# Performance work log

Measured on AMD Instinct MI355X. Metric: run time of the kernel, lower is better.

The kernel has to match this reference:

```python
import jax, jax.numpy as jnp
import numpy as np
import math

N_PATCH = 32768
DIM = 512
L_TOK = 64
W_SIZE = 64
STRIDE = 32


def setup_inputs() -> dict:
    key = jax.random.key(0)
    ks = jax.random.split(key, 12)
    d = DIM
    inp = {
        'feats': jax.random.normal(ks[0], (N_PATCH, d), dtype=jnp.float32),
        'coords': jax.random.uniform(ks[1], (N_PATCH, 2), dtype=jnp.float32),
        'mask': jnp.zeros((N_PATCH,), dtype=bool),
        'z': jax.random.normal(ks[2], (L_TOK, d), dtype=jnp.float32),
        'Wq': jax.random.normal(ks[3], (d, d), dtype=jnp.float32) / math.sqrt(d),
        'Wk': jax.random.normal(ks[4], (d, d), dtype=jnp.float32) / math.sqrt(d),
        'Wv': jax.random.normal(ks[5], (d, d), dtype=jnp.float32) / math.sqrt(d),
        'w1': jax.random.normal(ks[6], (d, 2), dtype=jnp.float32) / math.sqrt(2.0),
        'b1': jnp.zeros((d,), dtype=jnp.float32),
        'w2': jax.random.normal(ks[7], (d, d), dtype=jnp.float32) / math.sqrt(d),
        'b2': jnp.zeros((d,), dtype=jnp.float32),
        'Wo': jax.random.normal(ks[8], (d, d), dtype=jnp.float32) / math.sqrt(d),
        'bo': jnp.zeros((d,), dtype=jnp.float32),
    }
    return inp


def _lstcwa(feats, coords, z, Wq, Wk, Wv, w1, b1, w2, b2, Wo, bo):
    # mask is all-False -> feats kept as-is; N divisible by L -> equal segments
    N, D = feats.shape
    L = z.shape[0]
    n = N // L                       # patches per segment
    nwin = -(-n // STRIDE)           # windows per segment (ceil)

    # window offsets within a segment, [nwin, w]; last window truncated via mask
    off = jnp.arange(nwin)[:, None] * STRIDE + jnp.arange(W_SIZE)[None, :]
    valid = off < n                  # [nwin, w]
    idx = jnp.arange(L)[:, None, None] * n + jnp.minimum(off, n - 1)[None]  # [L,nwin,w]

    q = z @ Wq.T                     # [L, D]
    kf = feats @ Wk.T                # [N, D]
    vf = feats @ Wv.T

    k_win = kf[idx]                  # [L, nwin, w, D]
    v_win = vf[idx]
    c_win = coords[idx]              # [L, nwin, w, 2]

    vf32 = valid.astype(feats.dtype)                      # [nwin, w]
    cnt = vf32.sum(-1)                                    # [nwin]
    c_mean = jnp.einsum('lnwc,nw->lnc', c_win, vf32) / cnt[None, :, None]
    delta = (c_win - c_mean[:, :, None, :]) * vf32[None, :, :, None]

    pos = jax.nn.relu(delta @ w1.T + b1) @ w2.T + b2      # [L, nwin, w, D]
    k_win = k_win + pos

    logits = jnp.einsum('ld,lnwd->lnw', q, k_win) / math.sqrt(D)
    logits = jnp.where(valid[None], logits, -1e9)
    attn = jax.nn.softmax(logits, axis=-1)                # [L, nwin, w]

    z_win = jnp.einsum('lnw,lnwd->lnd', attn, v_win)      # [L, nwin, D]
    # return_alpha=False path: z_l_acc / max(1, len(attn_acc)=0) -> SUM over windows
    Z = z_win.sum(1)                                      # [L, D]
    return Z @ Wo.T + bo


def reference(feats, coords, mask, z, Wq, Wk, Wv, w1, b1, w2, b2, Wo, bo):
    # mask is all-False by construction (static shapes under jit)
    return _lstcwa(feats, coords, z, Wq, Wk, Wv, w1, b1, w2, b2, Wo, bo)
```

## Files before the change

kernel.cpp:

```cpp
#include <hip/hip_runtime.h>
#include <math.h>

#define DIMV 512
#define LTOK 64
#define SEG  512
#define NWIN 16
#define WSZ  64
#define INV_SQRT_D 0.044194173824159216f

__device__ __forceinline__ float wave_sum(float v) {
#pragma unroll
  for (int m = 1; m < 64; m <<= 1) v += __shfl_xor(v, m, 64);
  return v;
}

__global__ __launch_bounds__(256, 4) void k_q(const float* __restrict__ z,
    const float* __restrict__ Wq, const float* __restrict__ coords,
    float* __restrict__ q, float* __restrict__ cmean)
{
  int l = blockIdx.x >> 4, c = blockIdx.x & 15;
  int wave = threadIdx.x >> 6, lane = threadIdx.x & 63;
  int e0 = lane << 3;
  const float* zp = z + l * DIMV + e0;
  float x0[8];
  *(float4*)&x0[0] = *(const float4*)zp;
  *(float4*)&x0[4] = *(const float4*)(zp + 4);
  int d0 = c * 32 + wave * 8;
  float rf[8][8];
#pragma unroll
  for (int k = 0; k < 8; ++k) {
    const float* rp = Wq + (size_t)(d0 + k) * DIMV + e0;
    *(float4*)&rf[k][0] = *(const float4*)rp;
    *(float4*)&rf[k][4] = *(const float4*)(rp + 4);
  }
#pragma unroll
  for (int k = 0; k < 8; ++k) {
    float p = 0.f;
#pragma unroll
    for (int j = 0; j < 8; ++j) p = fmaf(rf[k][j], x0[j], p);
    p = wave_sum(p);
    if (lane == k) q[l * DIMV + d0 + k] = p;
  }
  if (wave == 0) {
    int n = c;
    int nvalid = (n == 15) ? 32 : 64;
    bool v = lane < nvalid;
    float cx = 0.f, cy = 0.f;
    if (v) {
      const float* cp = coords + ((size_t)(l * SEG + n * 32 + lane)) * 2;
      cx = cp[0]; cy = cp[1];
    }
    float inv = 1.0f / (float)nvalid;
    float mx = wave_sum(cx) * inv;
    float my = wave_sum(cy) * inv;
    if (lane == 0) {
      cmean[(l * NWIN + n) * 2]     = mx;
      cmean[(l * NWIN + n) * 2 + 1] = my;
    }
  }
}

__global__ __launch_bounds__(256) void k_qproj(const float* __restrict__ q,
    const float* __restrict__ Wk, const float* __restrict__ w2,
    const float* __restrict__ b2, float* __restrict__ qk,
    float* __restrict__ qw2, float* __restrict__ qb2)
{
  int l = blockIdx.x >> 3, ec = blockIdx.x & 7;
  int wave = threadIdx.x >> 6, lane = threadIdx.x & 63;
  int t = threadIdx.x;
  __shared__ float qs[DIMV];
  __shared__ float pk[4][64], pw[4][64];
  qs[t] = q[l * DIMV + t];
  qs[t + 256] = q[l * DIMV + t + 256];
  __syncthreads();
  int e = ec * 64 + lane;
  int d0 = wave * 128;
  float ak = 0.f, aw = 0.f;
#pragma unroll 8
  for (int dd = 0; dd < 128; ++dd) {
    int d = d0 + dd;
    float qd = qs[d];
    ak = fmaf(qd, Wk[(size_t)d * DIMV + e], ak);
    aw = fmaf(qd, w2[(size_t)d * DIMV + e], aw);
  }
  pk[wave][lane] = ak;
  pw[wave][lane] = aw;
  __syncthreads();
  if (wave == 0) {
    qk[l * DIMV + e] = pk[0][lane] + pk[1][lane] + pk[2][lane] + pk[3][lane];
  } else if (wave == 1) {
    qw2[l * DIMV + e] = pw[0][lane] + pw[1][lane] + pw[2][lane] + pw[3][lane];
  } else if (wave == 2 && ec == 0) {
    int e0 = lane << 3;
    float pb = 0.f;
#pragma unroll
    for (int j = 0; j < 8; ++j) pb = fmaf(qs[e0 + j], b2[e0 + j], pb);
    pb = wave_sum(pb);
    if (lane == 0) qb2[l] = pb;
  }
}

__global__ __launch_bounds__(256, 4) void k_pos(
    const float* __restrict__ coords, const float* __restrict__ cmean,
    const float* __restrict__ qw2,   const float* __restrict__ qb2,
    const float* __restrict__ w1,    const float* __restrict__ b1,
    float* __restrict__ pos)
{
  int widx = blockIdx.x;
  int l = widx >> 4, n = widx & 15;
  int t = threadIdx.x;
  int p = t & 63, qd = t >> 6;
  __shared__ float w1s[2 * DIMV], b1s[DIMV], qws[DIMV], part[4][WSZ];
#pragma unroll
  for (int i = 0; i < 4; ++i) w1s[t + 256 * i] = w1[t + 256 * i];
#pragma unroll
  for (int i = 0; i < 2; ++i) {
    b1s[t + 256 * i] = b1[t + 256 * i];
    qws[t + 256 * i] = qw2[l * DIMV + t + 256 * i];
  }
  __syncthreads();
  int nvalid = (n == 15) ? 32 : 64;
  int off = n * 32 + p;
  int row = (p < nvalid) ? off : (SEG - 1);
  float dx = coords[((size_t)(l * SEG + row)) * 2]     - cmean[(l * NWIN + n) * 2];
  float dy = coords[((size_t)(l * SEG + row)) * 2 + 1] - cmean[(l * NWIN + n) * 2 + 1];
  float acc = 0.f;
  int d0 = qd * 128;
#pragma unroll 4
  for (int dd = 0; dd < 128; ++dd) {
    int d = d0 + dd;
    float h = fmaf(dx, w1s[2 * d], fmaf(dy, w1s[2 * d + 1], b1s[d]));
    acc = fmaf(fmaxf(h, 0.f), qws[d], acc);
  }
  part[qd][p] = acc;
  __syncthreads();
  if (t < 64) {
    pos[(size_t)widx * WSZ + p] =
        part[0][p] + part[1][p] + part[2][p] + part[3][p] + qb2[l];
  }
}

__global__ __launch_bounds__(256, 4) void k_stream(
    const float* __restrict__ feats, const float* __restrict__ qk,
    const float* __restrict__ pos,   float* __restrict__ numA,
    float* __restrict__ numB, float* __restrict__ denA, float* __restrict__ denB)
{
  int bid = blockIdx.x;
  int swz = (bid & 7) * 128 + (bid >> 3);
  int l = swz >> 4, c = swz & 15;
  int wave = threadIdx.x >> 6, lane = threadIdx.x & 63;
  int col = lane << 2;
  int t = threadIdx.x;

  float4 qka = *(const float4*)(qk + l * DIMV + col);
  float4 qkb = *(const float4*)(qk + l * DIMV + 256 + col);
  const float* posA = pos + ((size_t)(l * NWIN) + c) * WSZ;
  const float* posB = pos + ((size_t)(l * NWIN) + (c > 0 ? c - 1 : 0)) * WSZ + 32;

  int rbase = c * 32 + wave * 8;
  const float* fbase = feats + ((size_t)(l * SEG + rbase)) * DIMV;

  float4 fa[8], fb[8];
#pragma unroll
  for (int k = 0; k < 8; ++k) {
    fa[k] = *(const float4*)(fbase + (size_t)k * DIMV + col);
    fb[k] = *(const float4*)(fbase + (size_t)k * DIMV + 256 + col);
  }

  float aA[8], aB[8];
#pragma unroll
  for (int j = 0; j < 8; ++j) { aA[j] = 0.f; aB[j] = 0.f; }
  float dA = 0.f, dB = 0.f;

#pragma unroll
  for (int k = 0; k < 8; ++k) {
    int rl = wave * 8 + k;
    float dot = fa[k].x * qka.x + fa[k].y * qka.y + fa[k].z * qka.z + fa[k].w * qka.w
              + fb[k].x * qkb.x + fb[k].y * qkb.y + fb[k].z * qkb.z + fb[k].w * qkb.w;
    dot = wave_sum(dot);
    float eh = __expf((dot + posA[rl]) * INV_SQRT_D);
    float el = (c > 0) ? __expf((dot + posB[rl]) * INV_SQRT_D) : 0.f;
    dA += eh; dB += el;
    aA[0] = fmaf(eh, fa[k].x, aA[0]); aA[1] = fmaf(eh, fa[k].y, aA[1]);
    aA[2] = fmaf(eh, fa[k].z, aA[2]); aA[3] = fmaf(eh, fa[k].w, aA[3]);
    aA[4] = fmaf(eh, fb[k].x, aA[4]); aA[5] = fmaf(eh, fb[k].y, aA[5]);
    aA[6] = fmaf(eh, fb[k].z, aA[6]); aA[7] = fmaf(eh, fb[k].w, aA[7]);
    aB[0] = fmaf(el, fa[k].x, aB[0]); aB[1] = fmaf(el, fa[k].y, aB[1]);
    aB[2] = fmaf(el, fa[k].z, aB[2]); aB[3] = fmaf(el, fa[k].w, aB[3]);
    aB[4] = fmaf(el, fb[k].x, aB[4]); aB[5] = fmaf(el, fb[k].y, aB[5]);
    aB[6] = fmaf(el, fb[k].z, aB[6]); aB[7] = fmaf(el, fb[k].w, aB[7]);
  }

  __shared__ float sA[4][DIMV], sB[4][DIMV];
  __shared__ float sd[4][2];
  *(float4*)&sA[wave][col]       = *(float4*)&aA[0];
  *(float4*)&sA[wave][256 + col] = *(float4*)&aA[4];
  *(float4*)&sB[wave][col]       = *(float4*)&aB[0];
  *(float4*)&sB[wave][256 + col] = *(float4*)&aB[4];
  if (lane == 0) { sd[wave][0] = dA; sd[wave][1] = dB; }
  __syncthreads();
  size_t ob = ((size_t)(l * NWIN) + c) * DIMV;
#pragma unroll
  for (int i = 0; i < 2; ++i) {
    int e = t + 256 * i;
    numA[ob + e] = sA[0][e] + sA[1][e] + sA[2][e] + sA[3][e];
    numB[ob + e] = sB[0][e] + sB[1][e] + sB[2][e] + sB[3][e];
  }
  if (t == 0) {
    denA[l * NWIN + c] = sd[0][0] + sd[1][0] + sd[2][0] + sd[3][0];
    denB[l * NWIN + c] = sd[0][1] + sd[1][1] + sd[2][1] + sd[3][1];
  }
}

__global__ __launch_bounds__(256, 4) void k_uv(
    const float* __restrict__ numA, const float* __restrict__ numB,
    const float* __restrict__ denA, const float* __restrict__ denB,
    const float* __restrict__ Wv,  float* __restrict__ tbuf)
{
  int bid = blockIdx.x;
  int swz = (bid & 7) * 128 + (bid >> 3);
  int l = swz >> 4, c = swz & 15;
  int wave = threadIdx.x >> 6, lane = threadIdx.x & 63;
  int e0 = lane << 3, t = threadIdx.x;
  __shared__ float us[DIMV];
  __shared__ float dinv[NWIN];
  if (t < NWIN) {
    float d = denA[l * NWIN + t];
    if (t < NWIN - 1) d += denB[l * NWIN + t + 1];
    dinv[t] = 1.0f / d;
  }
  __syncthreads();
#pragma unroll
  for (int i = 0; i < 2; ++i) {
    int e = t + 256 * i;
    float u = 0.f;
#pragma unroll
    for (int n = 0; n < NWIN; ++n) {
      float na = numA[((size_t)(l * NWIN) + n) * DIMV + e];
      if (n < NWIN - 1) na += numB[((size_t)(l * NWIN) + n + 1) * DIMV + e];
      u = fmaf(na, dinv[n], u);
    }
    us[e] = u;
  }
  __syncthreads();
  float x0[8];
  *(float4*)&x0[0] = *(float4*)&us[e0];
  *(float4*)&x0[4] = *(float4*)&us[e0 + 4];
  int f0 = c * 32 + wave * 8;
  float rf[8][8];
#pragma unroll
  for (int k = 0; k < 8; ++k) {
    const float* rp = Wv + (size_t)(f0 + k) * DIMV + e0;
    *(float4*)&rf[k][0] = *(const float4*)rp;
    *(float4*)&rf[k][4] = *(const float4*)(rp + 4);
  }
#pragma unroll
  for (int k = 0; k < 8; ++k) {
    float p = 0.f;
#pragma unroll
    for (int j = 0; j < 8; ++j) p = fmaf(rf[k][j], x0[j], p);
    p = wave_sum(p);
    if (lane == k) tbuf[l * DIMV + f0 + k] = p;
  }
}

__global__ __launch_bounds__(256, 4) void k_out(const float* __restrict__ tbuf,
    const float* __restrict__ Wo, const float* __restrict__ bo,
    float* __restrict__ out)
{
  int l = blockIdx.x >> 4, c = blockIdx.x & 15;
  int wave = threadIdx.x >> 6, lane = threadIdx.x & 63;
  int e0 = lane << 3;
  const float* tp = tbuf + l * DIMV + e0;
  float x0[8];
  *(float4*)&x0[0] = *(const float4*)tp;
  *(float4*)&x0[4] = *(const float4*)(tp + 4);
  int d0 = c * 32 + wave * 8;
  float rf[8][8];
#pragma unroll
  for (int k = 0; k < 8; ++k) {
    const float* rp = Wo + (size_t)(d0 + k) * DIMV + e0;
    *(float4*)&rf[k][0] = *(const float4*)rp;
    *(float4*)&rf[k][4] = *(const float4*)(rp + 4);
  }
#pragma unroll
  for (int k = 0; k < 8; ++k) {
    float p = 0.f;
#pragma unroll
    for (int j = 0; j < 8; ++j) p = fmaf(rf[k][j], x0[j], p);
    p = wave_sum(p);
    if (lane == k) out[l * DIMV + d0 + k] = p + bo[d0 + k];
  }
}

extern "C" void kernel_launch(void* const* d_in, const int* in_sizes, int n_in,
                              void* d_out, int out_size, void* d_ws, size_t ws_size,
                              hipStream_t stream) {
  (void)in_sizes; (void)n_in; (void)out_size; (void)ws_size;
  const float* feats  = (const float*)d_in[0];
  const float* coords = (const float*)d_in[1];
  const float* z   = (const float*)d_in[3];
  const float* Wq  = (const float*)d_in[4];
  const float* Wk  = (const float*)d_in[5];
  const float* Wv  = (const float*)d_in[6];
  const float* w1  = (const float*)d_in[7];
  const float* b1  = (const float*)d_in[8];
  const float* w2  = (const float*)d_in[9];
  const float* b2  = (const float*)d_in[10];
  const float* Wo  = (const float*)d_in[11];
  const float* bo  = (const float*)d_in[12];
  float* out = (float*)d_out;

  float* q     = (float*)d_ws;
  float* qk    = q     + LTOK * DIMV;
  float* qw2   = qk    + LTOK * DIMV;
  float* qb2   = qw2   + LTOK * DIMV;
  float* cmean = qb2   + LTOK;
  float* pos   = cmean + LTOK * NWIN * 2;
  float* numA  = pos   + LTOK * NWIN * WSZ;
  float* numB  = numA  + LTOK * NWIN * DIMV;
  float* denA  = numB  + LTOK * NWIN * DIMV;
  float* denB  = denA  + LTOK * NWIN;
  float* tbuf  = denB  + LTOK * NWIN;

  hipLaunchKernelGGL(k_q,      dim3(LTOK * NWIN), dim3(256), 0, stream,
                     z, Wq, coords, q, cmean);
  hipLaunchKernelGGL(k_qproj,  dim3(LTOK * 8),    dim3(256), 0, stream,
                     q, Wk, w2, b2, qk, qw2, qb2);
  hipLaunchKernelGGL(k_pos,    dim3(LTOK * NWIN), dim3(256), 0, stream,
                     coords, cmean, qw2, qb2, w1, b1, pos);
  hipLaunchKernelGGL(k_stream, dim3(LTOK * NWIN), dim3(256), 0, stream,
                     feats, qk, pos, numA, numB, denA, denB);
  hipLaunchKernelGGL(k_uv,     dim3(LTOK * NWIN), dim3(256), 0, stream,
                     numA, numB, denA, denB, Wv, tbuf);
  hipLaunchKernelGGL(k_out,    dim3(LTOK * NWIN), dim3(256), 0, stream,
                     tbuf, Wo, bo, out);
}
```

Baseline: 59.18 us.

## Drop LDS staging in qproj/pos, one wave per window, nontemporal feats loads

k_qproj now reads q directly through wave-uniform scalar loads instead of staging it in shared memory with a barrier. k_pos is restructured so each wave computes a whole window over all 512 hidden dims, which removes the shared-memory staging of w1/b1/qw2, the cross-wave reduction and both barriers, and launches a quarter as many blocks. k_stream loads feats with nontemporal hints to avoid polluting cache. The costs are longer serial loops per wave in k_pos and a dependence on the scalar cache for the broadcast weight loads.

```diff
diff --git a/kernel.cpp b/kernel.cpp
--- a/kernel.cpp
+++ b/kernel.cpp
@@ -7,6 +7,8 @@
 #define NWIN 16
 #define WSZ  64
 #define INV_SQRT_D 0.044194173824159216f
+
+typedef float f32x4 __attribute__((ext_vector_type(4)));
 
 __device__ __forceinline__ float wave_sum(float v) {
 #pragma unroll
@@ -66,22 +68,20 @@
     float* __restrict__ qw2, float* __restrict__ qb2)
 {
   int l = blockIdx.x >> 3, ec = blockIdx.x & 7;
-  int wave = threadIdx.x >> 6, lane = threadIdx.x & 63;
   int t = threadIdx.x;
-  __shared__ float qs[DIMV];
+  int lane = t & 63;
+  int wave = __builtin_amdgcn_readfirstlane(t >> 6);
   __shared__ float pk[4][64], pw[4][64];
-  qs[t] = q[l * DIMV + t];
-  qs[t + 256] = q[l * DIMV + t + 256];
-  __syncthreads();
   int e = ec * 64 + lane;
-  int d0 = wave * 128;
+  const float* qrow = q + l * DIMV + wave * 128;
+  const float* wkc  = Wk + (size_t)(wave * 128) * DIMV + e;
+  const float* w2c  = w2 + (size_t)(wave * 128) * DIMV + e;
   float ak = 0.f, aw = 0.f;
 #pragma unroll 8
   for (int dd = 0; dd < 128; ++dd) {
-    int d = d0 + dd;
-    float qd = qs[d];
-    ak = fmaf(qd, Wk[(size_t)d * DIMV + e], ak);
-    aw = fmaf(qd, w2[(size_t)d * DIMV + e], aw);
+    float qd = qrow[dd];
+    ak = fmaf(qd, wkc[(size_t)dd * DIMV], ak);
+    aw = fmaf(qd, w2c[(size_t)dd * DIMV], aw);
   }
   pk[wave][lane] = ak;
   pw[wave][lane] = aw;
@@ -92,52 +92,39 @@
     qw2[l * DIMV + e] = pw[0][lane] + pw[1][lane] + pw[2][lane] + pw[3][lane];
   } else if (wave == 2 && ec == 0) {
     int e0 = lane << 3;
+    const float* qp = q + l * DIMV + e0;
+    const float* bp = b2 + e0;
     float pb = 0.f;
 #pragma unroll
-    for (int j = 0; j < 8; ++j) pb = fmaf(qs[e0 + j], b2[e0 + j], pb);
+    for (int j = 0; j < 8; ++j) pb = fmaf(qp[j], bp[j], pb);
     pb = wave_sum(pb);
     if (lane == 0) qb2[l] = pb;
   }
 }
 
-__global__ __launch_bounds__(256, 4) void k_pos(
+__global__ __launch_bounds__(256) void k_pos(
     const float* __restrict__ coords, const float* __restrict__ cmean,
     const float* __restrict__ qw2,   const float* __restrict__ qb2,
     const float* __restrict__ w1,    const float* __restrict__ b1,
     float* __restrict__ pos)
 {
-  int widx = blockIdx.x;
+  int widx = __builtin_amdgcn_readfirstlane(blockIdx.x * 4 + (threadIdx.x >> 6));
+  int lane = threadIdx.x & 63;
   int l = widx >> 4, n = widx & 15;
-  int t = threadIdx.x;
-  int p = t & 63, qd = t >> 6;
-  __shared__ float w1s[2 * DIMV], b1s[DIMV], qws[DIMV], part[4][WSZ];
-#pragma unroll
-  for (int i = 0; i < 4; ++i) w1s[t + 256 * i] = w1[t + 256 * i];
-#pragma unroll
-  for (int i = 0; i < 2; ++i) {
-    b1s[t + 256 * i] = b1[t + 256 * i];
-    qws[t + 256 * i] = qw2[l * DIMV + t + 256 * i];
-  }
-  __syncthreads();
   int nvalid = (n == 15) ? 32 : 64;
-  int off = n * 32 + p;
-  int row = (p < nvalid) ? off : (SEG - 1);
+  int off = n * 32 + lane;
+  int row = (lane < nvalid) ? off : (SEG - 1);
   float dx = coords[((size_t)(l * SEG + row)) * 2]     - cmean[(l * NWIN + n) * 2];
   float dy = coords[((size_t)(l * SEG + row)) * 2 + 1] - cmean[(l * NWIN + n) * 2 + 1];
+  const float* qwp = qw2 + l * DIMV;
   float acc = 0.f;
-  int d0 = qd * 128;
-#pragma unroll 4
-  for (int dd = 0; dd < 128; ++dd) {
-    int d = d0 + dd;
-    float h = fmaf(dx, w1s[2 * d], fmaf(dy, w1s[2 * d + 1], b1s[d]));
-    acc = fmaf(fmaxf(h, 0.f), qws[d], acc);
-  }
-  part[qd][p] = acc;
-  __syncthreads();
-  if (t < 64) {
-    pos[(size_t)widx * WSZ + p] =
-        part[0][p] + part[1][p] + part[2][p] + part[3][p] + qb2[l];
-  }
+#pragma unroll 8
+  for (int d = 0; d < DIMV; ++d) {
+    float2 wv = *(const float2*)(w1 + 2 * d);
+    float h = fmaf(dx, wv.x, fmaf(dy, wv.y, b1[d]));
+    acc = fmaf(fmaxf(h, 0.f), qwp[d], acc);
+  }
+  pos[(size_t)widx * WSZ + lane] = acc + qb2[l];
 }
 
 __global__ __launch_bounds__(256, 4) void k_stream(
@@ -160,11 +147,11 @@
   int rbase = c * 32 + wave * 8;
   const float* fbase = feats + ((size_t)(l * SEG + rbase)) * DIMV;
 
-  float4 fa[8], fb[8];
-#pragma unroll
-  for (int k = 0; k < 8; ++k) {
-    fa[k] = *(const float4*)(fbase + (size_t)k * DIMV + col);
-    fb[k] = *(const float4*)(fbase + (size_t)k * DIMV + 256 + col);
+  f32x4 fa[8], fb[8];
+#pragma unroll
+  for (int k = 0; k < 8; ++k) {
+    fa[k] = __builtin_nontemporal_load((const f32x4*)(fbase + (size_t)k * DIMV + col));
+    fb[k] = __builtin_nontemporal_load((const f32x4*)(fbase + (size_t)k * DIMV + 256 + col));
   }
 
   float aA[8], aB[8];
@@ -323,16 +310,16 @@
   float* denB  = denA  + LTOK * NWIN;
   float* tbuf  = denB  + LTOK * NWIN;
 
-  hipLaunchKernelGGL(k_q,      dim3(LTOK * NWIN), dim3(256), 0, stream,
+  hipLaunchKernelGGL(k_q,      dim3(LTOK * NWIN),     dim3(256), 0, stream,
                      z, Wq, coords, q, cmean);
-  hipLaunchKernelGGL(k_qproj,  dim3(LTOK * 8),    dim3(256), 0, stream,
+  hipLaunchKernelGGL(k_qproj,  dim3(LTOK * 8),        dim3(256), 0, stream,
                      q, Wk, w2, b2, qk, qw2, qb2);
-  hipLaunchKernelGGL(k_pos,    dim3(LTOK * NWIN), dim3(256), 0, stream,
+  hipLaunchKernelGGL(k_pos,    dim3(LTOK * NWIN / 4), dim3(256), 0, stream,
                      coords, cmean, qw2, qb2, w1, b1, pos);
-  hipLaunchKernelGGL(k_stream, dim3(LTOK * NWIN), dim3(256), 0, stream,
+  hipLaunchKernelGGL(k_stream, dim3(LTOK * NWIN),     dim3(256), 0, stream,
                      feats, qk, pos, numA, numB, denA, denB);
-  hipLaunchKernelGGL(k_uv,     dim3(LTOK * NWIN), dim3(256), 0, stream,
+  hipLaunchKernelGGL(k_uv,     dim3(LTOK * NWIN),     dim3(256), 0, stream,
                      numA, numB, denA, denB, Wv, tbuf);
-  hipLaunchKernelGGL(k_out,    dim3(LTOK * NWIN), dim3(256), 0, stream,
+  hipLaunchKernelGGL(k_out,    dim3(LTOK * NWIN),     dim3(256), 0, stream,
                      tbuf, Wo, bo, out);
 }
```

After: 71.37 us. 1.21x slower.
